# Optimization experiments

Measured on AMD Instinct MI355X. Metric: run time of the kernel, lower is better.

The kernel has to match this reference:

```python
import jax, jax.numpy as jnp
import numpy as np

N_NODES = 100000
N_EDGES = 1600000
IN_DIM, HID_DIM, OUT_DIM = 128, 64, 40


def setup_inputs() -> dict:
    key = jax.random.key(0)
    k = jax.random.split(key, 6)
    feats = jax.random.normal(k[0], (N_NODES, IN_DIM), dtype=jnp.float32)
    src = jax.random.randint(k[1], (N_EDGES,), 0, N_NODES)
    dst = jax.random.randint(k[2], (N_EDGES,), 0, N_NODES)
    # Glorot-ish init for the two GraphConv weights
    W1 = jax.random.normal(k[3], (IN_DIM, HID_DIM), dtype=jnp.float32) * (2.0 / (IN_DIM + HID_DIM)) ** 0.5
    b1 = jnp.zeros((HID_DIM,), dtype=jnp.float32)
    W2 = jax.random.normal(k[4], (HID_DIM, OUT_DIM), dtype=jnp.float32) * (2.0 / (HID_DIM + OUT_DIM)) ** 0.5
    b2 = jnp.zeros((OUT_DIM,), dtype=jnp.float32)
    return {"feats": feats, "W1": W1, "b1": b1, "W2": W2, "b2": b2, "src": src, "dst": dst}


def _graph_conv(h, W, b, src, dst, n):
    # DGL GraphConv, norm='both': out = D_dst^{-1/2} * A^T * (D_src^{-1/2} * h) W + b
    # (weight applied before aggregation since in_feats > out_feats for both layers)
    ones_e = jnp.ones(src.shape, dtype=h.dtype)
    deg_out = jax.ops.segment_sum(ones_e, src, num_segments=n)
    deg_in = jax.ops.segment_sum(ones_e, dst, num_segments=n)
    norm_src = jnp.clip(deg_out, 1.0) ** -0.5  # [N]
    norm_dst = jnp.clip(deg_in, 1.0) ** -0.5   # [N]
    h = h * norm_src[:, None]
    h = h @ W                                   # [N, out]
    m = jax.ops.segment_sum(h[src], dst, num_segments=n)  # gather-scatter over edges
    return m * norm_dst[:, None] + b


def reference(feats, W1, b1, W2, b2, src, dst):
    n = feats.shape[0]
    # layer 0: GraphConv with relu activation (dropout is identity in eval)
    h1 = jax.nn.relu(_graph_conv(feats, W1, b1, src, dst, n))
    # layer 1: GraphConv, no activation
    h2 = _graph_conv(h1, W2, b2, src, dst, n)
    # GCN.forward returns (h_list, h); h_list holds the hidden layer output
    return (h1, h2)
```

## Files before the change

### kernel.cpp

```cpp
#include <hip/hip_runtime.h>
#include <hip/hip_bf16.h>

constexpr int N_NODES = 100000;
constexpr int N_EDGES = 1600000;
constexpr int IN_DIM  = 128;
constexpr int HID_DIM = 64;
constexpr int OUT_DIM = 40;

constexpr int BK_SHIFT = 9;
constexpr int NBKT = (N_NODES + 511) >> 9;
constexpr int ECAP = 9216;
constexpr int TILE = 2048;
constexpr int NTILES = (N_EDGES + TILE - 1) / TILE;
constexpr int GEMM_BLK = (N_NODES + 63) / 64;

typedef __attribute__((ext_vector_type(8))) short short8;
typedef __attribute__((ext_vector_type(4))) float f32x4;

__device__ inline float bf2f(unsigned int u16) {
  union { float f; unsigned int i; } c;
  c.i = u16 << 16;
  return c.f;
}

__device__ inline unsigned short f2bf(float f) {
  union { float f; unsigned int u; } c; c.f = f;
  unsigned int u = c.u + 0x7fffu + ((c.u >> 16) & 1u);
  return (unsigned short)(u >> 16);
}

__global__ void k_init(const float* __restrict__ W1, const float* __restrict__ W2,
                       unsigned short* __restrict__ Bfrag1, unsigned short* __restrict__ Bfrag2,
                       int* __restrict__ gcur) {
  int tid = threadIdx.x;
  for (int i = tid; i < 2 * NBKT; i += 256) gcur[i] = 0;
  for (int idx = tid; idx < 4 * 4 * 64 * 8; idx += 256) {
    int j = idx & 7;
    int lane = (idx >> 3) & 63;
    int nt = (idx >> 9) & 3;
    int ks = idx >> 11;
    int k = ks * 32 + 8 * (lane >> 4) + j;
    int col = nt * 16 + (lane & 15);
    Bfrag1[idx] = f2bf(W1[k * HID_DIM + col]);
  }
  for (int idx = tid; idx < 2 * 3 * 64 * 8; idx += 256) {
    int j = idx & 7;
    int lane = (idx >> 3) & 63;
    int nt = (idx >> 9) % 3;
    int ks = idx / (3 * 512);
    int k = ks * 32 + 8 * (lane >> 4) + j;
    int col = nt * 16 + (lane & 15);
    Bfrag2[idx] = (col < OUT_DIM) ? f2bf(W2[k * OUT_DIM + col]) : (unsigned short)0;
  }
}

__global__ __launch_bounds__(256) void k_part(const int* __restrict__ src,
                                              const int* __restrict__ dst,
                                              int* __restrict__ gcur,
                                              int* __restrict__ gcur2,
                                              unsigned int* __restrict__ pairs,
                                              unsigned short* __restrict__ spart) {
  __shared__ int scnt[NBKT], soff[NBKT], gbase[NBKT];
  __shared__ int scnt2[NBKT], soff2[NBKT], gbase2[NBKT];
  __shared__ int sc1[256], sc2[256];
  __shared__ unsigned int sord[TILE];
  __shared__ unsigned char sordB[TILE];
  __shared__ unsigned short sordS[TILE];
  __shared__ unsigned char sordSB[TILE];
  int tid = threadIdx.x;
  int tileBase = blockIdx.x * TILE;
  int tcnt = N_EDGES - tileBase; if (tcnt > TILE) tcnt = TILE;
  if (tid < NBKT) { scnt[tid] = 0; scnt2[tid] = 0; }
  __syncthreads();
  int s_[8], d_[8], pos_[8], pos2_[8];
#pragma unroll
  for (int t = 0; t < 8; ++t) {
    int idx = tileBase + t * 256 + tid;
    if (idx < N_EDGES) {
      s_[t] = src[idx];
      d_[t] = dst[idx];
      pos_[t]  = atomicAdd(&scnt[d_[t] >> BK_SHIFT], 1);
      pos2_[t] = atomicAdd(&scnt2[s_[t] >> BK_SHIFT], 1);
    }
  }
  __syncthreads();
  int v1 = (tid < NBKT) ? scnt[tid] : 0;
  int v2 = (tid < NBKT) ? scnt2[tid] : 0;
  sc1[tid] = v1; sc2[tid] = v2;
  __syncthreads();
  for (int o = 1; o < 256; o <<= 1) {
    int x1 = (tid >= o) ? sc1[tid - o] : 0;
    int x2 = (tid >= o) ? sc2[tid - o] : 0;
    __syncthreads();
    sc1[tid] += x1; sc2[tid] += x2;
    __syncthreads();
  }
  if (tid < NBKT) {
    soff[tid]  = sc1[tid] - v1;
    soff2[tid] = sc2[tid] - v2;
    gbase[tid]  = v1 ? atomicAdd(&gcur[tid],  v1) : 0;
    gbase2[tid] = v2 ? atomicAdd(&gcur2[tid], v2) : 0;
  }
  __syncthreads();
#pragma unroll
  for (int t = 0; t < 8; ++t) {
    int idx = tileBase + t * 256 + tid;
    if (idx < N_EDGES) {
      int b  = d_[t] >> BK_SHIFT;
      int b2 = s_[t] >> BK_SHIFT;
      int p  = soff[b] + pos_[t];
      int p2 = soff2[b2] + pos2_[t];
      sord[p]  = (unsigned)s_[t] | ((unsigned)(d_[t] & 511) << 17);
      sordB[p] = (unsigned char)b;
      sordS[p2]  = (unsigned short)(s_[t] & 511);
      sordSB[p2] = (unsigned char)b2;
    }
  }
  __syncthreads();
  for (int i = tid; i < tcnt; i += 256) {
    int b = sordB[i];
    int g = gbase[b] + (i - soff[b]);
    if (g < ECAP) pairs[(size_t)b * ECAP + g] = sord[i];
  }
  for (int i = tid; i < tcnt; i += 256) {
    int b = sordSB[i];
    int g = gbase2[b] + (i - soff2[b]);
    if (g < ECAP) spart[(size_t)b * ECAP + g] = sordS[i];
  }
}

__global__ __launch_bounds__(256) void k_csrdeg(const unsigned int* __restrict__ pairs,
                                                const unsigned short* __restrict__ spart,
                                                const int* __restrict__ gcur,
                                                const int* __restrict__ gcur2,
                                                int* __restrict__ startg,
                                                int* __restrict__ cntg,
                                                float* __restrict__ norm_dst,
                                                float* __restrict__ norm_src,
                                                int* __restrict__ esrc) {
  __shared__ int cnt[512];
  __shared__ int off[512];
  __shared__ int cur[512];
  __shared__ int wsum[256];
  __shared__ int esrcL[ECAP];
  int tid = threadIdx.x;
  if (blockIdx.x >= NBKT) {
    int b = blockIdx.x - NBKT;
    int node0 = b << BK_SHIFT;
    int nNodes = N_NODES - node0; if (nNodes > 512) nNodes = 512;
    int E = gcur2[b]; if (E > ECAP) E = ECAP;
    cnt[tid] = 0; cnt[tid + 256] = 0;
    __syncthreads();
    const unsigned short* sp = spart + (size_t)b * ECAP;
    for (int i = tid; i < E; i += 256) atomicAdd(&cnt[sp[i]], 1);
    __syncthreads();
    for (int j = tid; j < nNodes; j += 256) {
      int c = cnt[j];
      norm_src[node0 + j] = rsqrtf((float)(c < 1 ? 1 : c));
    }
    return;
  }
  int b = blockIdx.x;
  int node0 = b << BK_SHIFT;
  int nNodes = N_NODES - node0; if (nNodes > 512) nNodes = 512;
  int E = gcur[b]; if (E > ECAP) E = ECAP;
  cnt[tid] = 0; cnt[tid + 256] = 0;
  __syncthreads();
  const unsigned int* pp = pairs + (size_t)b * ECAP;
  for (int i = tid; i < E; i += 256) atomicAdd(&cnt[pp[i] >> 17], 1);
  __syncthreads();
  int v0 = cnt[tid * 2], v1 = cnt[tid * 2 + 1];
  int s = v0 + v1;
  wsum[tid] = s; __syncthreads();
  for (int o = 1; o < 256; o <<= 1) {
    int x = (tid >= o) ? wsum[tid - o] : 0;
    __syncthreads();
    wsum[tid] += x;
    __syncthreads();
  }
  int excl = wsum[tid] - s;
  off[tid * 2] = excl;     cur[tid * 2] = excl;
  off[tid * 2 + 1] = excl + v0; cur[tid * 2 + 1] = excl + v0;
  __syncthreads();
  for (int i = tid; i < E; i += 256) {
    unsigned p = pp[i];
    int pos = atomicAdd(&cur[p >> 17], 1);
    esrcL[pos] = (int)(p & 0x1FFFFu);
  }
  __syncthreads();
  int base = b * ECAP;
  for (int i = tid; i < E; i += 256) esrc[base + i] = esrcL[i];
  for (int j = tid; j < nNodes; j += 256) {
    int c = cnt[j];
    startg[node0 + j] = base + off[j];
    cntg[node0 + j] = c;
    norm_dst[node0 + j] = rsqrtf((float)(c < 1 ? 1 : c));
  }
}

__global__ __launch_bounds__(256) void k_gemm1_mfma(
    const float* __restrict__ feats, const uint4* __restrict__ Bfrag1,
    const float* __restrict__ norm_src, __hip_bfloat16* __restrict__ t1) {
  int tid = threadIdx.x;
  int w = tid >> 6, lane = tid & 63;
  int row0 = blockIdx.x * 64 + w * 16;
  int arow = row0 + (lane & 15);
  int arowc = arow < N_NODES ? arow : N_NODES - 1;
  int half = lane >> 4;

  const float4* fr = (const float4*)(feats + (size_t)arowc * IN_DIM);
  f32x4 acc[4] = {{0.f,0.f,0.f,0.f},{0.f,0.f,0.f,0.f},{0.f,0.f,0.f,0.f},{0.f,0.f,0.f,0.f}};
#pragma unroll
  for (int ks = 0; ks < 4; ++ks) {
    float4 p0 = fr[ks * 8 + 2 * half];
    float4 p1 = fr[ks * 8 + 2 * half + 1];
    short8 a;
    a[0] = (short)f2bf(p0.x); a[1] = (short)f2bf(p0.y);
    a[2] = (short)f2bf(p0.z); a[3] = (short)f2bf(p0.w);
    a[4] = (short)f2bf(p1.x); a[5] = (short)f2bf(p1.y);
    a[6] = (short)f2bf(p1.z); a[7] = (short)f2bf(p1.w);
#pragma unroll
    for (int nt = 0; nt < 4; ++nt) {
      uint4 bu = Bfrag1[(ks * 4 + nt) * 64 + lane];
      short8 b = *(const short8*)&bu;
      acc[nt] = __builtin_amdgcn_mfma_f32_16x16x32_bf16(a, b, acc[nt], 0, 0, 0);
    }
  }
  int col = lane & 15;
  int rbase = row0 + half * 4;
#pragma unroll
  for (int r = 0; r < 4; ++r) {
    int grow = rbase + r;
    if (grow < N_NODES) {
      float ns = norm_src[grow];
#pragma unroll
      for (int nt = 0; nt < 4; ++nt) {
        unsigned short h = f2bf(acc[nt][r] * ns);
        *((unsigned short*)t1 + (size_t)grow * HID_DIM + nt * 16 + col) = h;
      }
    }
  }
}

__global__ __launch_bounds__(256) void k_agg1g2(
    const uint2* __restrict__ t1, const int* __restrict__ startg,
    const int* __restrict__ cntg, const int* __restrict__ esrc,
    const float* __restrict__ norm_dst, const float* __restrict__ norm_src,
    const float4* __restrict__ b1, const uint4* __restrict__ Bfrag2,
    float4* __restrict__ out1, __hip_bfloat16* __restrict__ t2) {
  __shared__ unsigned short h1s[16][64];
  int tid = threadIdx.x;
  int g = tid >> 4, q = tid & 15;
  int n = blockIdx.x * 16 + g;
  int s0 = startg[n];
  int c  = cntg[n];
  const int* bk = esrc + s0;
  float a0 = 0.f, a1 = 0.f, a2 = 0.f, a3 = 0.f;
  for (int i = 0; i < c; i += 8) {
#pragma unroll
    for (int t = 0; t < 8; ++t) {
      int ii = i + t;
      bool ok = ii < c;
      int s = bk[ok ? ii : 0];
      uint2 v = t1[(size_t)s * 16 + q];
      unsigned vx = ok ? v.x : 0u;
      unsigned vy = ok ? v.y : 0u;
      a0 += bf2f(vx & 0xffffu);
      a1 += bf2f(vx >> 16);
      a2 += bf2f(vy & 0xffffu);
      a3 += bf2f(vy >> 16);
    }
  }
  float nd = norm_dst[n];
  float4 bb = b1[q];
  float h0 = fmaxf(a0 * nd + bb.x, 0.f);
  float h1 = fmaxf(a1 * nd + bb.y, 0.f);
  float h2 = fmaxf(a2 * nd + bb.z, 0.f);
  float h3 = fmaxf(a3 * nd + bb.w, 0.f);
  out1[(size_t)n * 16 + q] = make_float4(h0, h1, h2, h3);
  float ns = norm_src[n];
  unsigned lo = (unsigned)f2bf(h0 * ns) | ((unsigned)f2bf(h1 * ns) << 16);
  unsigned hi = (unsigned)f2bf(h2 * ns) | ((unsigned)f2bf(h3 * ns) << 16);
  *(uint2*)&h1s[g][q * 4] = make_uint2(lo, hi);
  __syncthreads();
  if (tid < 64) {
    int lane = tid;
    int r = lane & 15, half = lane >> 4;
    f32x4 acc[3] = {{0.f,0.f,0.f,0.f},{0.f,0.f,0.f,0.f},{0.f,0.f,0.f,0.f}};
#pragma unroll
    for (int ks = 0; ks < 2; ++ks) {
      short8 a = *(const short8*)&h1s[r][ks * 32 + 8 * half];
#pragma unroll
      for (int nt = 0; nt < 3; ++nt) {
        uint4 bu = Bfrag2[(ks * 3 + nt) * 64 + lane];
        short8 b = *(const short8*)&bu;
        acc[nt] = __builtin_amdgcn_mfma_f32_16x16x32_bf16(a, b, acc[nt], 0, 0, 0);
      }
    }
    int col = lane & 15;
#pragma unroll
    for (int r2 = 0; r2 < 4; ++r2) {
      int node = blockIdx.x * 16 + half * 4 + r2;
#pragma unroll
      for (int nt = 0; nt < 3; ++nt) {
        int j = nt * 16 + col;
        if (j < OUT_DIM)
          *((unsigned short*)t2 + (size_t)node * OUT_DIM + j) = f2bf(acc[nt][r2]);
      }
    }
  }
}

__global__ __launch_bounds__(256) void k_agg2(
    const uint2* __restrict__ t2, const int* __restrict__ startg,
    const int* __restrict__ cntg, const int* __restrict__ esrc,
    const float* __restrict__ norm_dst, const float4* __restrict__ b2,
    float4* __restrict__ out2) {
  int idx = blockIdx.x * blockDim.x + threadIdx.x;
  int n = idx / 10;
  int q = idx - n * 10;
  if (n >= N_NODES) return;
  int s0 = startg[n];
  int c  = cntg[n];
  const int* bk = esrc + s0;
  float a0 = 0.f, a1 = 0.f, a2 = 0.f, a3 = 0.f;
  for (int i = 0; i < c; i += 8) {
#pragma unroll
    for (int t = 0; t < 8; ++t) {
      int ii = i + t;
      bool ok = ii < c;
      int s = bk[ok ? ii : 0];
      uint2 v = t2[(size_t)s * 10 + q];
      unsigned vx = ok ? v.x : 0u;
      unsigned vy = ok ? v.y : 0u;
      a0 += bf2f(vx & 0xffffu);
      a1 += bf2f(vx >> 16);
      a2 += bf2f(vy & 0xffffu);
      a3 += bf2f(vy >> 16);
    }
  }
  float nd = norm_dst[n];
  float4 bb = b2[q];
  float4 r;
  r.x = a0 * nd + bb.x;
  r.y = a1 * nd + bb.y;
  r.z = a2 * nd + bb.z;
  r.w = a3 * nd + bb.w;
  out2[(size_t)n * 10 + q] = r;
}

extern "C" void kernel_launch(void* const* d_in, const int* in_sizes, int n_in,
                              void* d_out, int out_size, void* d_ws, size_t ws_size,
                              hipStream_t stream) {
  const float* feats = (const float*)d_in[0];
  const float* W1    = (const float*)d_in[1];
  const float* b1    = (const float*)d_in[2];
  const float* W2    = (const float*)d_in[3];
  const float* b2    = (const float*)d_in[4];
  const int*   src   = (const int*)d_in[5];
  const int*   dst   = (const int*)d_in[6];

  float* out  = (float*)d_out;
  float* out1 = out;
  float* out2 = out + (size_t)N_NODES * HID_DIM;

  __hip_bfloat16* t1 = (__hip_bfloat16*)d_ws;
  __hip_bfloat16* t2 = t1 + (size_t)N_NODES * HID_DIM;
  unsigned int* pairs = (unsigned int*)(t2 + (size_t)N_NODES * OUT_DIM);
  unsigned short* spart = (unsigned short*)(pairs + (size_t)NBKT * ECAP);
  int* esrc   = (int*)(spart + (size_t)NBKT * ECAP);
  unsigned short* Bfrag1 = (unsigned short*)(esrc + (size_t)NBKT * ECAP);
  unsigned short* Bfrag2 = Bfrag1 + 4 * 4 * 64 * 8;
  int* startg = (int*)(Bfrag2 + 2 * 3 * 64 * 8);
  int* cntg   = startg + N_NODES;
  float* norm_src = (float*)(cntg + N_NODES);
  float* norm_dst = norm_src + N_NODES;
  int* gcur  = (int*)(norm_dst + N_NODES);
  int* gcur2 = gcur + NBKT;

  k_init<<<1, 256, 0, stream>>>(W1, W2, Bfrag1, Bfrag2, gcur);
  k_part<<<NTILES, 256, 0, stream>>>(src, dst, gcur, gcur2, pairs, spart);
  k_csrdeg<<<2 * NBKT, 256, 0, stream>>>(pairs, spart, gcur, gcur2,
                                         startg, cntg, norm_dst, norm_src, esrc);

  k_gemm1_mfma<<<GEMM_BLK, 256, 0, stream>>>(feats, (const uint4*)Bfrag1, norm_src, t1);
  k_agg1g2<<<N_NODES / 16, 256, 0, stream>>>((const uint2*)t1, startg, cntg, esrc,
                                             norm_dst, norm_src, (const float4*)b1,
                                             (const uint4*)Bfrag2, (float4*)out1, t2);
  k_agg2<<<(N_NODES * 10 + 255) / 256, 256, 0, stream>>>((const uint2*)t2, startg, cntg, esrc,
                                                         norm_dst, (const float4*)b2, (float4*)out2);
}
```

Measured before the change: 147.8 us.

## Sort nodes by in-degree within buckets to balance aggregation work

```diff
diff --git a/kernel.cpp b/kernel.cpp
--- a/kernel.cpp
+++ b/kernel.cpp
@@ -10,7 +10,8 @@
 constexpr int BK_SHIFT = 9;
 constexpr int NBKT = (N_NODES + 511) >> 9;
 constexpr int ECAP = 9216;
-constexpr int TILE = 2048;
+constexpr int TILE = 4096;
+constexpr int EPT  = TILE / 256;
 constexpr int NTILES = (N_EDGES + TILE - 1) / TILE;
 constexpr int GEMM_BLK = (N_NODES + 63) / 64;
 
@@ -32,9 +33,10 @@
 __global__ void k_init(const float* __restrict__ W1, const float* __restrict__ W2,
                        unsigned short* __restrict__ Bfrag1, unsigned short* __restrict__ Bfrag2,
                        int* __restrict__ gcur) {
-  int tid = threadIdx.x;
-  for (int i = tid; i < 2 * NBKT; i += 256) gcur[i] = 0;
-  for (int idx = tid; idx < 4 * 4 * 64 * 8; idx += 256) {
+  int tid = blockIdx.x * blockDim.x + threadIdx.x;
+  int stride = gridDim.x * blockDim.x;
+  for (int i = tid; i < 2 * NBKT; i += stride) gcur[i] = 0;
+  for (int idx = tid; idx < 4 * 4 * 64 * 8; idx += stride) {
     int j = idx & 7;
     int lane = (idx >> 3) & 63;
     int nt = (idx >> 9) & 3;
@@ -43,7 +45,7 @@
     int col = nt * 16 + (lane & 15);
     Bfrag1[idx] = f2bf(W1[k * HID_DIM + col]);
   }
-  for (int idx = tid; idx < 2 * 3 * 64 * 8; idx += 256) {
+  for (int idx = tid; idx < 2 * 3 * 64 * 8; idx += stride) {
     int j = idx & 7;
     int lane = (idx >> 3) & 63;
     int nt = (idx >> 9) % 3;
@@ -72,9 +74,9 @@
   int tcnt = N_EDGES - tileBase; if (tcnt > TILE) tcnt = TILE;
   if (tid < NBKT) { scnt[tid] = 0; scnt2[tid] = 0; }
   __syncthreads();
-  int s_[8], d_[8], pos_[8], pos2_[8];
-#pragma unroll
-  for (int t = 0; t < 8; ++t) {
+  int s_[EPT], d_[EPT], pos_[EPT], pos2_[EPT];
+#pragma unroll
+  for (int t = 0; t < EPT; ++t) {
     int idx = tileBase + t * 256 + tid;
     if (idx < N_EDGES) {
       s_[t] = src[idx];
@@ -103,7 +105,7 @@
   }
   __syncthreads();
 #pragma unroll
-  for (int t = 0; t < 8; ++t) {
+  for (int t = 0; t < EPT; ++t) {
     int idx = tileBase + t * 256 + tid;
     if (idx < N_EDGES) {
       int b  = d_[t] >> BK_SHIFT;
@@ -137,11 +139,13 @@
                                                 int* __restrict__ cntg,
                                                 float* __restrict__ norm_dst,
                                                 float* __restrict__ norm_src,
-                                                int* __restrict__ esrc) {
+                                                int* __restrict__ esrc,
+                                                int* __restrict__ permG) {
   __shared__ int cnt[512];
   __shared__ int off[512];
   __shared__ int cur[512];
   __shared__ int wsum[256];
+  __shared__ int dh[64], dcur[64];
   __shared__ int esrcL[ECAP];
   int tid = threadIdx.x;
   if (blockIdx.x >= NBKT) {
@@ -165,6 +169,7 @@
   int nNodes = N_NODES - node0; if (nNodes > 512) nNodes = 512;
   int E = gcur[b]; if (E > ECAP) E = ECAP;
   cnt[tid] = 0; cnt[tid + 256] = 0;
+  if (tid < 64) dh[tid] = 0;
   __syncthreads();
   const unsigned int* pp = pairs + (size_t)b * ECAP;
   for (int i = tid; i < E; i += 256) atomicAdd(&cnt[pp[i] >> 17], 1);
@@ -187,14 +192,24 @@
     int pos = atomicAdd(&cur[p >> 17], 1);
     esrcL[pos] = (int)(p & 0x1FFFFu);
   }
-  __syncthreads();
+  for (int j = tid; j < nNodes; j += 256) {
+    int c = cnt[j]; atomicAdd(&dh[c < 63 ? c : 63], 1);
+  }
+  __syncthreads();
+  if (tid == 0) {
+    int acc = 0;
+    for (int i = 0; i < 64; ++i) { int c = dh[i]; dcur[i] = acc; acc += c; }
+  }
   int base = b * ECAP;
   for (int i = tid; i < E; i += 256) esrc[base + i] = esrcL[i];
+  __syncthreads();
   for (int j = tid; j < nNodes; j += 256) {
     int c = cnt[j];
     startg[node0 + j] = base + off[j];
     cntg[node0 + j] = c;
     norm_dst[node0 + j] = rsqrtf((float)(c < 1 ? 1 : c));
+    int p = atomicAdd(&dcur[c < 63 ? c : 63], 1);
+    permG[node0 + p] = node0 + j;
   }
 }
 
@@ -245,13 +260,16 @@
 __global__ __launch_bounds__(256) void k_agg1g2(
     const uint2* __restrict__ t1, const int* __restrict__ startg,
     const int* __restrict__ cntg, const int* __restrict__ esrc,
+    const int* __restrict__ permG,
     const float* __restrict__ norm_dst, const float* __restrict__ norm_src,
     const float4* __restrict__ b1, const uint4* __restrict__ Bfrag2,
     float4* __restrict__ out1, __hip_bfloat16* __restrict__ t2) {
   __shared__ unsigned short h1s[16][64];
+  __shared__ int nodes[16];
   int tid = threadIdx.x;
   int g = tid >> 4, q = tid & 15;
-  int n = blockIdx.x * 16 + g;
+  int n = permG[blockIdx.x * 16 + g];
+  if (q == 0) nodes[g] = n;
   int s0 = startg[n];
   int c  = cntg[n];
   const int* bk = esrc + s0;
@@ -300,7 +318,7 @@
     int col = lane & 15;
 #pragma unroll
     for (int r2 = 0; r2 < 4; ++r2) {
-      int node = blockIdx.x * 16 + half * 4 + r2;
+      int node = nodes[half * 4 + r2];
 #pragma unroll
       for (int nt = 0; nt < 3; ++nt) {
         int j = nt * 16 + col;
@@ -314,12 +332,14 @@
 __global__ __launch_bounds__(256) void k_agg2(
     const uint2* __restrict__ t2, const int* __restrict__ startg,
     const int* __restrict__ cntg, const int* __restrict__ esrc,
+    const int* __restrict__ permG,
     const float* __restrict__ norm_dst, const float4* __restrict__ b2,
     float4* __restrict__ out2) {
   int idx = blockIdx.x * blockDim.x + threadIdx.x;
-  int n = idx / 10;
-  int q = idx - n * 10;
-  if (n >= N_NODES) return;
+  int slot = idx / 10;
+  int q = idx - slot * 10;
+  if (slot >= N_NODES) return;
+  int n = permG[slot];
   int s0 = startg[n];
   int c  = cntg[n];
   const int* bk = esrc + s0;
@@ -375,18 +395,19 @@
   int* cntg   = startg + N_NODES;
   float* norm_src = (float*)(cntg + N_NODES);
   float* norm_dst = norm_src + N_NODES;
-  int* gcur  = (int*)(norm_dst + N_NODES);
+  int* permG = (int*)(norm_dst + N_NODES);
+  int* gcur  = permG + N_NODES;
   int* gcur2 = gcur + NBKT;
 
-  k_init<<<1, 256, 0, stream>>>(W1, W2, Bfrag1, Bfrag2, gcur);
+  k_init<<<16, 256, 0, stream>>>(W1, W2, Bfrag1, Bfrag2, gcur);
   k_part<<<NTILES, 256, 0, stream>>>(src, dst, gcur, gcur2, pairs, spart);
   k_csrdeg<<<2 * NBKT, 256, 0, stream>>>(pairs, spart, gcur, gcur2,
-                                         startg, cntg, norm_dst, norm_src, esrc);
+                                         startg, cntg, norm_dst, norm_src, esrc, permG);
 
   k_gemm1_mfma<<<GEMM_BLK, 256, 0, stream>>>(feats, (const uint4*)Bfrag1, norm_src, t1);
-  k_agg1g2<<<N_NODES / 16, 256, 0, stream>>>((const uint2*)t1, startg, cntg, esrc,
+  k_agg1g2<<<N_NODES / 16, 256, 0, stream>>>((const uint2*)t1, startg, cntg, esrc, permG,
                                              norm_dst, norm_src, (const float4*)b1,
                                              (const uint4*)Bfrag2, (float4*)out1, t2);
-  k_agg2<<<(N_NODES * 10 + 255) / 256, 256, 0, stream>>>((const uint2*)t2, startg, cntg, esrc,
+  k_agg2<<<(N_NODES * 10 + 255) / 256, 256, 0, stream>>>((const uint2*)t2, startg, cntg, esrc, permG,
                                                          norm_dst, (const float4*)b2, (float4*)out2);
 }
```

New measurement: 147.8 us. No clear change (-0.0%).
